# Kernel optimization log

Hardware: AMD Instinct MI355X
Metric: run time of the kernel (lower is better)

## Reference

```python
import jax, jax.numpy as jnp
import numpy as np

IN_FEATURES = 3
HIDDEN = 32
NUM_LAYERS = 3
BATCH = 16384
NQ = 128


def setup_inputs() -> dict:
    key = jax.random.key(0)
    ks = jax.random.split(key, 12)
    x = jax.random.normal(ks[0], (BATCH, NQ, IN_FEATURES), dtype=jnp.float32)
    # adjacency with self-loops, row-normalised so each row sums to 1
    a = jax.random.uniform(ks[1], (NQ, NQ), dtype=jnp.float32)
    a = a + jnp.eye(NQ, dtype=jnp.float32)
    adj = a / jnp.sum(a, axis=1, keepdims=True)
    s_lift = 1.0 / np.sqrt(IN_FEATURES)
    s_hid = 1.0 / np.sqrt(HIDDEN)
    W_lift = jax.random.uniform(ks[2], (IN_FEATURES, HIDDEN), jnp.float32, -s_lift, s_lift)
    b_lift = jax.random.uniform(ks[3], (HIDDEN,), jnp.float32, -s_lift, s_lift)
    # stacked per-layer MLP params: [num_layers, ...]
    W1 = jax.random.uniform(ks[4], (NUM_LAYERS, HIDDEN, HIDDEN), jnp.float32, -s_hid, s_hid)
    b1 = jax.random.uniform(ks[5], (NUM_LAYERS, HIDDEN), jnp.float32, -s_hid, s_hid)
    W2 = jax.random.uniform(ks[6], (NUM_LAYERS, HIDDEN, HIDDEN), jnp.float32, -s_hid, s_hid)
    b2 = jax.random.uniform(ks[7], (NUM_LAYERS, HIDDEN), jnp.float32, -s_hid, s_hid)
    W_ro = jax.random.uniform(ks[8], (HIDDEN, 1), jnp.float32, -s_hid, s_hid)
    b_ro = jax.random.uniform(ks[9], (1,), jnp.float32, -s_hid, s_hid)
    return {"x": x, "adj": adj, "W_lift": W_lift, "b_lift": b_lift,
            "W1": W1, "b1": b1, "W2": W2, "b2": b2,
            "W_ro": W_ro, "b_ro": b_ro}


def reference(x, adj, W_lift, b_lift, W1, b1, W2, b2, W_ro, b_ro):
    # lift: [B, N, in] -> [B, N, H]
    h = x @ W_lift + b_lift
    for l in range(W1.shape[0]):  # small fixed layer count
        # local MLP: Linear -> ReLU -> (Dropout: identity at eval) -> Linear
        local = jnp.maximum(h @ W1[l] + b1[l], 0.0) @ W2[l] + b2[l]
        # dense adjacency aggregation: [N,N] x [B,N,H] -> [B,N,H]
        h = jnp.einsum('ij,bjk->bik', adj, local)
    graph_repr = jnp.mean(h, axis=1)  # [B, H]
    return graph_repr @ W_ro + b_ro   # [B, 1]
```

## Files before the change

### kernel.cpp

```cpp
#include <hip/hip_runtime.h>


typedef _Float16 f16;
typedef __attribute__((ext_vector_type(8))) _Float16 half8;
typedef __attribute__((ext_vector_type(4))) _Float16 half4;
typedef __attribute__((ext_vector_type(2))) __fp16 fp16x2;
typedef __attribute__((ext_vector_type(4))) float f32x4;

namespace {
constexpr int N = 128, H = 32;
constexpr int WS_ADJB = 0;
constexpr int WS_W0B  = 32768;
constexpr int WS_MB   = 33792;
constexpr int WS_BIAS = 37888;
constexpr int WS_V    = 38400;
constexpr int WS_U    = 38912;
constexpr int WS_C    = 39040;
}

static __device__ __forceinline__ half4 pk4(float a, float b, float c, float d) {
  union { half4 v; fp16x2 h[2]; } u;
  u.h[0] = __builtin_amdgcn_cvt_pkrtz(a, b);
  u.h[1] = __builtin_amdgcn_cvt_pkrtz(c, d);
  return u.v;
}
static __device__ __forceinline__ half4 relupk(f32x4 c) {
  const half4 z = {};
  return __builtin_elementwise_max(pk4(c[0], c[1], c[2], c[3]), z);
}
static __device__ __forceinline__ half4 pkc(f32x4 c) {
  return pk4(c[0], c[1], c[2], c[3]);
}
static __device__ __forceinline__ half8 cat(half4 lo, half4 hi) {
  return __builtin_shufflevector(lo, hi, 0, 1, 2, 3, 4, 5, 6, 7);
}

#define MF(A, B, C)   __builtin_amdgcn_mfma_f32_16x16x16f16((A), (B), (C), 0, 0, 0)
#define MF32(A, B, C) __builtin_amdgcn_mfma_f32_16x16x32_f16((A), (B), (C), 0, 0, 0)

__global__ void prep(const float* __restrict__ adj,
                     const float* __restrict__ W_lift,
                     const float* __restrict__ b_lift,
                     const float* __restrict__ W1,
                     const float* __restrict__ b1,
                     const float* __restrict__ W2,
                     const float* __restrict__ b2,
                     const float* __restrict__ W_ro,
                     const float* __restrict__ b_ro,
                     char* __restrict__ ws) {
  const int tid = threadIdx.x;
  f16* adjb  = (f16*)(ws + WS_ADJB);
  f16* w0b   = (f16*)(ws + WS_W0B);
  f16* mb    = (f16*)(ws + WS_MB);
  float* bia = (float*)(ws + WS_BIAS);
  float* v   = (float*)(ws + WS_V);
  float* u   = (float*)(ws + WS_U);
  float* cp  = (float*)(ws + WS_C);

  if (blockIdx.x != 0) {
    const int e = (blockIdx.x - 1) * 256 + tid;
    const int gi = e >> 8, c = (e >> 6) & 3, lane = e & 63;
    const int lr = lane & 15, q = lane >> 4;
    const float* src = adj + (gi * 16 + lr) * N + c * 32;
    f16* dst = adjb + e * 8;
#pragma unroll
    for (int j = 0; j < 8; ++j) {
      const int col = (j < 4) ? (4 * q + j) : (12 + 4 * q + j);
      dst[j] = (f16)src[col];
    }
    return;
  }

  __shared__ float tmp[3][H][H];
  __shared__ float vpart[2][N];
  {
    const int c = tid & 127, h = tid >> 7;
    float s = 0.f;
    for (int i = h * 64; i < h * 64 + 64; ++i) s += adj[i * N + c];
    vpart[h][c] = s;
  }
  for (int idx = tid; idx < 3 * H * H; idx += 256) {
    const int l = idx >> 10, rem = idx & 1023;
    const int k = rem >> 5, fo = rem & 31;
    float val = 0.f;
    if (l == 0) {
      if (k < 3) for (int c = 0; c < H; ++c) val += W_lift[k * H + c] * W1[c * H + fo];
    } else {
      const float* w2l = W2 + (l - 1) * H * H;
      const float* w1n = W1 + l * H * H;
      for (int c = 0; c < H; ++c) val += w2l[k * H + c] * w1n[c * H + fo];
    }
    tmp[l][k][fo] = val;
  }
  if (tid < H) {
    float s0 = b1[tid], s1 = b1[H + tid], s2 = b1[2 * H + tid];
    for (int c = 0; c < H; ++c) {
      s0 += b_lift[c] * W1[c * H + tid];
      s1 += b2[c] * W1[H * H + c * H + tid];
      s2 += b2[H + c] * W1[2 * H * H + c * H + tid];
    }
    bia[tid] = s0; bia[H + tid] = s1; bia[2 * H + tid] = s2;
    float su = 0.f;
    for (int c = 0; c < H; ++c) su += W2[2 * H * H + tid * H + c] * W_ro[c];
    u[tid] = su;
  }
  __syncthreads();
  if (tid < N) v[tid] = (vpart[0][tid] + vpart[1][tid]) * (1.0f / N);
  for (int e = tid; e < 512; e += 256) {
    const int t = e >> 8, lane = (e >> 2) & 63, j = e & 3;
    const int lr = lane & 15, q = lane >> 4;
    w0b[e] = (f16)tmp[0][q * 4 + j][t * 16 + lr];
  }
  for (int e = tid; e < 2048; e += 256) {
    const int l = e >> 10, rem = e & 1023;
    const int t = rem >> 9, lane = (rem >> 3) & 63, j = rem & 7;
    const int lr = lane & 15, q = lane >> 4;
    const int k = (j < 4) ? (4 * q + j) : (12 + 4 * q + j);
    mb[e] = (f16)tmp[1 + l][k][t * 16 + lr];
  }
  __syncthreads();
  if (tid < 64) {
    float s = (vpart[0][tid] + vpart[1][tid] + vpart[0][64 + tid] + vpart[1][64 + tid])
              * (1.0f / N);
#pragma unroll
    for (int off = 32; off > 0; off >>= 1) s += __shfl_down(s, off, 64);
    if (tid == 0) {
      float c2r = 0.f;
      for (int k = 0; k < H; ++k) c2r += b2[2 * H + k] * W_ro[k];
      cp[0] = c2r * s + b_ro[0];
    }
  }
}

__global__ __launch_bounds__(256, 2)
void gnn_mfma(const float* __restrict__ x,
              const char* __restrict__ ws,
              float* __restrict__ out) {
  const f16* adjb  = (const f16*)(ws + WS_ADJB);
  const f16* w0b   = (const f16*)(ws + WS_W0B);
  const f16* mb    = (const f16*)(ws + WS_MB);
  const float* bia = (const float*)(ws + WS_BIAS);
  const float* v   = (const float*)(ws + WS_V);
  const float* u   = (const float*)(ws + WS_U);
  const float* cp  = (const float*)(ws + WS_C);

  const int tid  = threadIdx.x;
  const int wave = tid >> 6;
  const int lane = tid & 63;
  const int lrow = lane & 15;
  const int quad = lane >> 4;
  const int b    = blockIdx.x * 4 + wave;

  const f32x4 zero = {0.f, 0.f, 0.f, 0.f};

  half8 ca0, ca1, ca2, ca3, cb0, cb1, cb2, cb3;
  half8 pf0, pf1, pf2, pf3, pf4, pf5, pf6, pf7;

  {
    const half4 w0 = *(const half4*)(w0b + (0 * 64 + lane) * 4);
    const half4 w1 = *(const half4*)(w0b + (1 * 64 + lane) * 4);
    const float bb0 = bia[lrow], bb1 = bia[16 + lrow];
    const f32x4 bi0 = {bb0, bb0, bb0, bb0};
    const f32x4 bi1 = {bb1, bb1, bb1, bb1};
#define L0PAIR(g, CA, CB)                                                    \
    {                                                                        \
      half4 xa0 = {}, xa1 = {};                                              \
      if (quad == 0) {                                                       \
        const float* xr0 = x + ((size_t)b * N + (g) * 16 + lrow) * 3;        \
        const float* xr1 = x + ((size_t)b * N + ((g) + 1) * 16 + lrow) * 3;  \
        xa0 = pk4(xr0[0], xr0[1], xr0[2], 0.f);                              \
        xa1 = pk4(xr1[0], xr1[1], xr1[2], 0.f);                              \
      }                                                                      \
      CA = cat(relupk(MF(xa0, w0, bi0)), relupk(MF(xa1, w0, bi0)));          \
      CB = cat(relupk(MF(xa0, w1, bi1)), relupk(MF(xa1, w1, bi1)));          \
    }
    L0PAIR(0, ca0, cb0) L0PAIR(2, ca1, cb1) L0PAIR(4, ca2, cb2) L0PAIR(6, ca3, cb3)
#undef L0PAIR
  }

#define GSTEP(gi, PF)                                                        \
  {                                                                          \
    f32x4 a0 = zero, a1 = zero;                                              \
    const f16* ab = adjb + ((gi) * 256 + lane) * 8;                          \
    half8 bt;                                                                \
    __builtin_amdgcn_s_setprio(1);                                           \
    bt = *(const half8*)(ab + 0 * 512);                                      \
    a0 = MF32(ca0, bt, a0); a1 = MF32(cb0, bt, a1);                          \
    bt = *(const half8*)(ab + 1 * 512);                                      \
    a0 = MF32(ca1, bt, a0); a1 = MF32(cb1, bt, a1);                          \
    bt = *(const half8*)(ab + 2 * 512);                                      \
    a0 = MF32(ca2, bt, a0); a1 = MF32(cb2, bt, a1);                          \
    bt = *(const half8*)(ab + 3 * 512);                                      \
    a0 = MF32(ca3, bt, a0); a1 = MF32(cb3, bt, a1);                          \
    __builtin_amdgcn_s_setprio(0);                                           \
    PF = cat(pkc(a0), pkc(a1));                                              \
  }
#define GALL()                                                               \
  GSTEP(0, pf0) GSTEP(1, pf1)                                                \
  __builtin_amdgcn_sched_barrier(0);                                         \
  GSTEP(2, pf2) GSTEP(3, pf3)                                                \
  __builtin_amdgcn_sched_barrier(0);                                         \
  GSTEP(4, pf4) GSTEP(5, pf5)                                                \
  __builtin_amdgcn_sched_barrier(0);                                         \
  GSTEP(6, pf6) GSTEP(7, pf7)

  GALL()

  {
    const f16* mbl = mb + 0 * 1024;
    const half8 m0 = *(const half8*)(mbl + (0 * 64 + lane) * 8);
    const half8 m1 = *(const half8*)(mbl + (1 * 64 + lane) * 8);
    const float bb0 = bia[H + lrow], bb1 = bia[H + 16 + lrow];
    const f32x4 bi0 = {bb0, bb0, bb0, bb0};
    const f32x4 bi1 = {bb1, bb1, bb1, bb1};
#define L1PAIR(PFA, PFB, CA, CB)                                             \
    {                                                                        \
      f32x4 c0a = MF32(PFA, m0, bi0);                                        \
      f32x4 c1a = MF32(PFA, m1, bi1);                                        \
      f32x4 c0b = MF32(PFB, m0, bi0);                                        \
      f32x4 c1b = MF32(PFB, m1, bi1);                                        \
      CA = cat(relupk(c0a), relupk(c0b));                                    \
      CB = cat(relupk(c1a), relupk(c1b));                                    \
    }
    L1PAIR(pf0, pf1, ca0, cb0) L1PAIR(pf2, pf3, ca1, cb1)
    __builtin_amdgcn_sched_barrier(0);
    L1PAIR(pf4, pf5, ca2, cb2) L1PAIR(pf6, pf7, ca3, cb3)
#undef L1PAIR
  }

  GALL()
#undef GALL
#undef GSTEP

  {
    const f16* mbl = mb + 1 * 1024;
    const half8 m0 = *(const half8*)(mbl + (0 * 64 + lane) * 8);
    const half8 m1 = *(const half8*)(mbl + (1 * 64 + lane) * 8);
    const float bb0 = bia[2 * H + lrow], bb1 = bia[2 * H + 16 + lrow];
    const f32x4 bi0 = {bb0, bb0, bb0, bb0};
    const f32x4 bi1 = {bb1, bb1, bb1, bb1};
    const float u0 = u[lrow], u1 = u[16 + lrow];
    float partial = 0.f;
#define L2G(g, PF)                                                           \
    {                                                                        \
      f32x4 c0 = MF32(PF, m0, bi0);                                          \
      f32x4 c1 = MF32(PF, m1, bi1);                                          \
      const float4 vv = *(const float4*)(v + (g) * 16 + quad * 4);           \
      partial += (fmaxf(c0[0], 0.f) * vv.x + fmaxf(c0[1], 0.f) * vv.y +      \
                  fmaxf(c0[2], 0.f) * vv.z + fmaxf(c0[3], 0.f) * vv.w) * u0 +\
                 (fmaxf(c1[0], 0.f) * vv.x + fmaxf(c1[1], 0.f) * vv.y +      \
                  fmaxf(c1[2], 0.f) * vv.z + fmaxf(c1[3], 0.f) * vv.w) * u1; \
    }
    L2G(0, pf0) L2G(1, pf1) L2G(2, pf2) L2G(3, pf3)
    L2G(4, pf4) L2G(5, pf5) L2G(6, pf6) L2G(7, pf7)
#undef L2G
#pragma unroll
    for (int off = 32; off > 0; off >>= 1) partial += __shfl_down(partial, off, 64);
    if (lane == 0) out[b] = partial + cp[0];
  }
}

extern "C" void kernel_launch(void* const* d_in, const int* in_sizes, int n_in,
                              void* d_out, int out_size, void* d_ws, size_t ws_size,
                              hipStream_t stream) {
  const float* x      = (const float*)d_in[0];
  const float* adj    = (const float*)d_in[1];
  const float* W_lift = (const float*)d_in[2];
  const float* b_lift = (const float*)d_in[3];
  const float* W1     = (const float*)d_in[4];
  const float* b1     = (const float*)d_in[5];
  const float* W2     = (const float*)d_in[6];
  const float* b2     = (const float*)d_in[7];
  const float* W_ro   = (const float*)d_in[8];
  const float* b_ro   = (const float*)d_in[9];
  char* ws = (char*)d_ws;
  float* o = (float*)d_out;

  const int B = in_sizes[0] / (N * 3);
  hipLaunchKernelGGL(prep, dim3(9), dim3(256), 0, stream,
                     adj, W_lift, b_lift, W1, b1, W2, b2, W_ro, b_ro, ws);
  hipLaunchKernelGGL(gnn_mfma, dim3(B / 4), dim3(256), 0, stream,
                     x, (const char*)ws, o);
}
```

Measured before the change: 139.5 us.

## Process two graphs per wavefront to reuse adjacency fragment loads

Each wavefront now handles two batch elements instead of one, so every adjacency B-fragment loaded in the aggregation step feeds four MFMAs instead of two, and the grid is halved. The aim is to cut adjacency load traffic per graph and raise MFMA density per load. In exchange the live register set roughly doubles (two sets of activations and partial features), which risks spills or lower occupancy under launch_bounds(256,2) and leaves fewer blocks to spread across CUs.

Result: no change. 138.0 us (-1.1%).

```diff
diff --git a/kernel.cpp b/kernel.cpp
--- a/kernel.cpp
+++ b/kernel.cpp
@@ -149,12 +149,15 @@
   const int lane = tid & 63;
   const int lrow = lane & 15;
   const int quad = lane >> 4;
-  const int b    = blockIdx.x * 4 + wave;
+  const int b0   = blockIdx.x * 8 + wave * 2;
+  const int b1   = b0 + 1;
 
   const f32x4 zero = {0.f, 0.f, 0.f, 0.f};
 
-  half8 ca0, ca1, ca2, ca3, cb0, cb1, cb2, cb3;
-  half8 pf0, pf1, pf2, pf3, pf4, pf5, pf6, pf7;
+  half8 caA0, caA1, caA2, caA3, cbA0, cbA1, cbA2, cbA3;
+  half8 caB0, caB1, caB2, caB3, cbB0, cbB1, cbB2, cbB3;
+  half8 pfA0, pfA1, pfA2, pfA3, pfA4, pfA5, pfA6, pfA7;
+  half8 pfB0, pfB1, pfB2, pfB3, pfB4, pfB5, pfB6, pfB7;
 
   {
     const half4 w0 = *(const half4*)(w0b + (0 * 64 + lane) * 4);
@@ -162,47 +165,59 @@
     const float bb0 = bia[lrow], bb1 = bia[16 + lrow];
     const f32x4 bi0 = {bb0, bb0, bb0, bb0};
     const f32x4 bi1 = {bb1, bb1, bb1, bb1};
-#define L0PAIR(g, CA, CB)                                                    \
+#define L0PAIR(g, CAA, CBA, CAB, CBB)                                        \
     {                                                                        \
-      half4 xa0 = {}, xa1 = {};                                              \
+      half4 xA0 = {}, xA1 = {}, xB0 = {}, xB1 = {};                          \
       if (quad == 0) {                                                       \
-        const float* xr0 = x + ((size_t)b * N + (g) * 16 + lrow) * 3;        \
-        const float* xr1 = x + ((size_t)b * N + ((g) + 1) * 16 + lrow) * 3;  \
-        xa0 = pk4(xr0[0], xr0[1], xr0[2], 0.f);                              \
-        xa1 = pk4(xr1[0], xr1[1], xr1[2], 0.f);                              \
+        const float* ra0 = x + ((size_t)b0 * N + (g) * 16 + lrow) * 3;       \
+        const float* ra1 = x + ((size_t)b0 * N + ((g) + 1) * 16 + lrow) * 3; \
+        const float* rb0 = x + ((size_t)b1 * N + (g) * 16 + lrow) * 3;       \
+        const float* rb1 = x + ((size_t)b1 * N + ((g) + 1) * 16 + lrow) * 3; \
+        xA0 = pk4(ra0[0], ra0[1], ra0[2], 0.f);                              \
+        xA1 = pk4(ra1[0], ra1[1], ra1[2], 0.f);                              \
+        xB0 = pk4(rb0[0], rb0[1], rb0[2], 0.f);                              \
+        xB1 = pk4(rb1[0], rb1[1], rb1[2], 0.f);                              \
       }                                                                      \
-      CA = cat(relupk(MF(xa0, w0, bi0)), relupk(MF(xa1, w0, bi0)));          \
-      CB = cat(relupk(MF(xa0, w1, bi1)), relupk(MF(xa1, w1, bi1)));          \
-    }
-    L0PAIR(0, ca0, cb0) L0PAIR(2, ca1, cb1) L0PAIR(4, ca2, cb2) L0PAIR(6, ca3, cb3)
+      CAA = cat(relupk(MF(xA0, w0, bi0)), relupk(MF(xA1, w0, bi0)));         \
+      CBA = cat(relupk(MF(xA0, w1, bi1)), relupk(MF(xA1, w1, bi1)));         \
+      CAB = cat(relupk(MF(xB0, w0, bi0)), relupk(MF(xB1, w0, bi0)));         \
+      CBB = cat(relupk(MF(xB0, w1, bi1)), relupk(MF(xB1, w1, bi1)));         \
+    }
+    L0PAIR(0, caA0, cbA0, caB0, cbB0) L0PAIR(2, caA1, cbA1, caB1, cbB1)
+    L0PAIR(4, caA2, cbA2, caB2, cbB2) L0PAIR(6, caA3, cbA3, caB3, cbB3)
 #undef L0PAIR
   }
 
-#define GSTEP(gi, PF)                                                        \
+#define GSTEP(gi, PFA, PFB)                                                  \
   {                                                                          \
-    f32x4 a0 = zero, a1 = zero;                                              \
+    f32x4 aA0 = zero, aA1 = zero, aB0 = zero, aB1 = zero;                    \
     const f16* ab = adjb + ((gi) * 256 + lane) * 8;                          \
     half8 bt;                                                                \
     __builtin_amdgcn_s_setprio(1);                                           \
     bt = *(const half8*)(ab + 0 * 512);                                      \
-    a0 = MF32(ca0, bt, a0); a1 = MF32(cb0, bt, a1);                          \
+    aA0 = MF32(caA0, bt, aA0); aA1 = MF32(cbA0, bt, aA1);                    \
+    aB0 = MF32(caB0, bt, aB0); aB1 = MF32(cbB0, bt, aB1);                    \
     bt = *(const half8*)(ab + 1 * 512);                                      \
-    a0 = MF32(ca1, bt, a0); a1 = MF32(cb1, bt, a1);                          \
+    aA0 = MF32(caA1, bt, aA0); aA1 = MF32(cbA1, bt, aA1);                    \
+    aB0 = MF32(caB1, bt, aB0); aB1 = MF32(cbB1, bt, aB1);                    \
     bt = *(const half8*)(ab + 2 * 512);                                      \
-    a0 = MF32(ca2, bt, a0); a1 = MF32(cb2, bt, a1);                          \
+    aA0 = MF32(caA2, bt, aA0); aA1 = MF32(cbA2, bt, aA1);                    \
+    aB0 = MF32(caB2, bt, aB0); aB1 = MF32(cbB2, bt, aB1);                    \
     bt = *(const half8*)(ab + 3 * 512);                                      \
-    a0 = MF32(ca3, bt, a0); a1 = MF32(cb3, bt, a1);                          \
+    aA0 = MF32(caA3, bt, aA0); aA1 = MF32(cbA3, bt, aA1);                    \
+    aB0 = MF32(caB3, bt, aB0); aB1 = MF32(cbB3, bt, aB1);                    \
     __builtin_amdgcn_s_setprio(0);                                           \
-    PF = cat(pkc(a0), pkc(a1));                                              \
+    PFA = cat(pkc(aA0), pkc(aA1));                                           \
+    PFB = cat(pkc(aB0), pkc(aB1));                                           \
   }
 #define GALL()                                                               \
-  GSTEP(0, pf0) GSTEP(1, pf1)                                                \
+  GSTEP(0, pfA0, pfB0) GSTEP(1, pfA1, pfB1)                                  \
   __builtin_amdgcn_sched_barrier(0);                                         \
-  GSTEP(2, pf2) GSTEP(3, pf3)                                                \
+  GSTEP(2, pfA2, pfB2) GSTEP(3, pfA3, pfB3)                                  \
   __builtin_amdgcn_sched_barrier(0);                                         \
-  GSTEP(4, pf4) GSTEP(5, pf5)                                                \
+  GSTEP(4, pfA4, pfB4) GSTEP(5, pfA5, pfB5)                                  \
   __builtin_amdgcn_sched_barrier(0);                                         \
-  GSTEP(6, pf6) GSTEP(7, pf7)
+  GSTEP(6, pfA6, pfB6) GSTEP(7, pfA7, pfB7)
 
   GALL()
 
@@ -213,18 +228,22 @@
     const float bb0 = bia[H + lrow], bb1 = bia[H + 16 + lrow];
     const f32x4 bi0 = {bb0, bb0, bb0, bb0};
     const f32x4 bi1 = {bb1, bb1, bb1, bb1};
-#define L1PAIR(PFA, PFB, CA, CB)                                             \
+#define L1PAIR(PF0, PF1, CA, CB)                                             \
     {                                                                        \
-      f32x4 c0a = MF32(PFA, m0, bi0);                                        \
-      f32x4 c1a = MF32(PFA, m1, bi1);                                        \
-      f32x4 c0b = MF32(PFB, m0, bi0);                                        \
-      f32x4 c1b = MF32(PFB, m1, bi1);                                        \
+      f32x4 c0a = MF32(PF0, m0, bi0);                                        \
+      f32x4 c1a = MF32(PF0, m1, bi1);                                        \
+      f32x4 c0b = MF32(PF1, m0, bi0);                                        \
+      f32x4 c1b = MF32(PF1, m1, bi1);                                        \
       CA = cat(relupk(c0a), relupk(c0b));                                    \
       CB = cat(relupk(c1a), relupk(c1b));                                    \
     }
-    L1PAIR(pf0, pf1, ca0, cb0) L1PAIR(pf2, pf3, ca1, cb1)
+    L1PAIR(pfA0, pfA1, caA0, cbA0) L1PAIR(pfB0, pfB1, caB0, cbB0)
     __builtin_amdgcn_sched_barrier(0);
-    L1PAIR(pf4, pf5, ca2, cb2) L1PAIR(pf6, pf7, ca3, cb3)
+    L1PAIR(pfA2, pfA3, caA1, cbA1) L1PAIR(pfB2, pfB3, caB1, cbB1)
+    __builtin_amdgcn_sched_barrier(0);
+    L1PAIR(pfA4, pfA5, caA2, cbA2) L1PAIR(pfB4, pfB5, caB2, cbB2)
+    __builtin_amdgcn_sched_barrier(0);
+    L1PAIR(pfA6, pfA7, caA3, cbA3) L1PAIR(pfB6, pfB7, caB3, cbB3)
 #undef L1PAIR
   }
 
@@ -240,23 +259,31 @@
     const f32x4 bi0 = {bb0, bb0, bb0, bb0};
     const f32x4 bi1 = {bb1, bb1, bb1, bb1};
     const float u0 = u[lrow], u1 = u[16 + lrow];
-    float partial = 0.f;
-#define L2G(g, PF)                                                           \
+    float pA = 0.f, pB = 0.f;
+#define L2G(g, PF, ACC)                                                      \
     {                                                                        \
       f32x4 c0 = MF32(PF, m0, bi0);                                          \
       f32x4 c1 = MF32(PF, m1, bi1);                                          \
       const float4 vv = *(const float4*)(v + (g) * 16 + quad * 4);           \
-      partial += (fmaxf(c0[0], 0.f) * vv.x + fmaxf(c0[1], 0.f) * vv.y +      \
-                  fmaxf(c0[2], 0.f) * vv.z + fmaxf(c0[3], 0.f) * vv.w) * u0 +\
-                 (fmaxf(c1[0], 0.f) * vv.x + fmaxf(c1[1], 0.f) * vv.y +      \
-                  fmaxf(c1[2], 0.f) * vv.z + fmaxf(c1[3], 0.f) * vv.w) * u1; \
-    }
-    L2G(0, pf0) L2G(1, pf1) L2G(2, pf2) L2G(3, pf3)
-    L2G(4, pf4) L2G(5, pf5) L2G(6, pf6) L2G(7, pf7)
+      ACC += (fmaxf(c0[0], 0.f) * vv.x + fmaxf(c0[1], 0.f) * vv.y +          \
+              fmaxf(c0[2], 0.f) * vv.z + fmaxf(c0[3], 0.f) * vv.w) * u0 +    \
+             (fmaxf(c1[0], 0.f) * vv.x + fmaxf(c1[1], 0.f) * vv.y +          \
+              fmaxf(c1[2], 0.f) * vv.z + fmaxf(c1[3], 0.f) * vv.w) * u1;     \
+    }
+    L2G(0, pfA0, pA) L2G(0, pfB0, pB) L2G(1, pfA1, pA) L2G(1, pfB1, pB)
+    L2G(2, pfA2, pA) L2G(2, pfB2, pB) L2G(3, pfA3, pA) L2G(3, pfB3, pB)
+    L2G(4, pfA4, pA) L2G(4, pfB4, pB) L2G(5, pfA5, pA) L2G(5, pfB5, pB)
+    L2G(6, pfA6, pA) L2G(6, pfB6, pB) L2G(7, pfA7, pA) L2G(7, pfB7, pB)
 #undef L2G
 #pragma unroll
-    for (int off = 32; off > 0; off >>= 1) partial += __shfl_down(partial, off, 64);
-    if (lane == 0) out[b] = partial + cp[0];
+    for (int off = 32; off > 0; off >>= 1) {
+      pA += __shfl_down(pA, off, 64);
+      pB += __shfl_down(pB, off, 64);
+    }
+    if (lane == 0) {
+      out[b0] = pA + cp[0];
+      out[b1] = pB + cp[0];
+    }
   }
 }
 
@@ -279,6 +306,6 @@
   const int B = in_sizes[0] / (N * 3);
   hipLaunchKernelGGL(prep, dim3(9), dim3(256), 0, stream,
                      adj, W_lift, b_lift, W1, b1, W2, b2, W_ro, b_ro, ws);
-  hipLaunchKernelGGL(gnn_mfma, dim3(B / 4), dim3(256), 0, stream,
+  hipLaunchKernelGGL(gnn_mfma, dim3(B / 8), dim3(256), 0, stream,
                      x, (const char*)ws, o);
 }
```
